# Kernel tuning notes

Hardware: AMD Instinct MI355X
Metric: run time of the kernel (lower is better)

## Reference

```python
import jax, jax.numpy as jnp
import numpy as np

VOCAB = 100000
EMBED = 128
B = 16384
W = 10  # context window size (indices fed as 'target' arg, per original naming)
K = 10  # number of negative samples


def setup_inputs() -> dict:
    key = jax.random.key(0)
    k1, k2, k3, k4 = jax.random.split(key, 4)
    initrange = 1.0 / EMBED
    # targetEmbedding: uniform(-1/D, 1/D); contextEmbedding: zeros (as in __init__).
    # Use small random values for contextEmbedding too so gradients/scores are non-trivial,
    # matching a mid-training state; math is identical.
    target_table = jax.random.uniform(k1, (VOCAB, EMBED), jnp.float32, -initrange, initrange)
    context_table = jax.random.uniform(k2, (VOCAB, EMBED), jnp.float32, -initrange, initrange)
    context = jax.random.randint(k3, (B,), 0, VOCAB)
    target = jax.random.randint(k4, (B, W), 0, VOCAB)
    negatives = jax.random.randint(jax.random.fold_in(key, 7), (B, K), 0, VOCAB)
    return {
        "target_table": target_table,
        "context_table": context_table,
        "context": context,
        "target": target,
        "negatives": negatives,
    }


def reference(target_table, context_table, context, target, negatives):
    # trg_embedding: gather window words then mean over window -> [B, D]
    trg = jnp.mean(target_table[target], axis=1)
    # center word embedding -> [B, D]
    ctx = context_table[context]
    # negatives embeddings -> [B, K, D]
    neg = context_table[negatives]

    pos_score = jnp.sum(trg * ctx, axis=1)                    # [B]
    pos_score = jnp.clip(pos_score, -10.0, 10.0)
    pos_loss = -jax.nn.log_sigmoid(pos_score)                 # [B]

    neg_score = jnp.einsum("bkd,bd->bk", neg, trg)           # [B, K]
    neg_score = jnp.clip(neg_score, -10.0, 10.0)
    neg_loss = -jnp.sum(jax.nn.log_sigmoid(-neg_score), axis=1)  # [B]

    return jnp.mean(pos_loss + neg_loss)
```

## Files before the change

### kernel.cpp

```cpp
#include <hip/hip_runtime.h>

#define VOCAB 100000
#define EMBED 128
#define BATCH 16384
#define WIN 10
#define NEG 10

__global__ __launch_bounds__(256) void cbow_loss_kernel(
    const float* __restrict__ target_table,
    const float* __restrict__ context_table,
    const int*   __restrict__ context,
    const int*   __restrict__ target,
    const int*   __restrict__ negatives,
    float*       __restrict__ out)
{
    const int tid    = threadIdx.x;
    const int lane16 = tid & 15;
    const int grp    = tid >> 4;
    const int b      = blockIdx.x * 16 + grp;

    const float4* tt4 = reinterpret_cast<const float4*>(target_table);
    const float4* ct4 = reinterpret_cast<const float4*>(context_table);
    const int lo = lane16 * 2;

    int tidx[WIN];
    #pragma unroll
    for (int w = 0; w < WIN; ++w) tidx[w] = target[b * WIN + w];
    const int cidx = context[b];
    int nidx[NEG];
    #pragma unroll
    for (int k = 0; k < NEG; ++k) nidx[k] = negatives[b * NEG + k];

    float4 t0 = make_float4(0.f, 0.f, 0.f, 0.f);
    float4 t1 = make_float4(0.f, 0.f, 0.f, 0.f);
    #pragma unroll
    for (int w = 0; w < WIN; ++w) {
        const float4* r = tt4 + (long long)tidx[w] * (EMBED / 4) + lo;
        const float4 a = r[0];
        const float4 c = r[1];
        t0.x += a.x; t0.y += a.y; t0.z += a.z; t0.w += a.w;
        t1.x += c.x; t1.y += c.y; t1.z += c.z; t1.w += c.w;
    }
    const float s = 1.0f / WIN;
    t0.x *= s; t0.y *= s; t0.z *= s; t0.w *= s;
    t1.x *= s; t1.y *= s; t1.z *= s; t1.w *= s;

    float sc[1 + NEG];
    {
        const float4* r = ct4 + (long long)cidx * (EMBED / 4) + lo;
        const float4 a = r[0];
        const float4 c = r[1];
        sc[0] = fmaf(t0.x, a.x, fmaf(t0.y, a.y, fmaf(t0.z, a.z, fmaf(t0.w, a.w,
                fmaf(t1.x, c.x, fmaf(t1.y, c.y, fmaf(t1.z, c.z, t1.w * c.w)))))));
    }
    #pragma unroll
    for (int k = 0; k < NEG; ++k) {
        const float4* r = ct4 + (long long)nidx[k] * (EMBED / 4) + lo;
        const float4 a = r[0];
        const float4 c = r[1];
        sc[1 + k] = fmaf(t0.x, a.x, fmaf(t0.y, a.y, fmaf(t0.z, a.z, fmaf(t0.w, a.w,
                    fmaf(t1.x, c.x, fmaf(t1.y, c.y, fmaf(t1.z, c.z, t1.w * c.w)))))));
    }

    #pragma unroll
    for (int off = 8; off >= 1; off >>= 1) {
        #pragma unroll
        for (int i = 0; i < 1 + NEG; ++i) sc[i] += __shfl_xor(sc[i], off, 16);
    }

    __shared__ float bsum;
    if (tid == 0) bsum = 0.f;
    __syncthreads();

    if (lane16 == 0) {
        float x = fminf(fmaxf(sc[0], -10.f), 10.f);
        float loss = log1pf(expf(-x));
        #pragma unroll
        for (int k = 0; k < NEG; ++k) {
            float y = fminf(fmaxf(sc[1 + k], -10.f), 10.f);
            loss += log1pf(expf(y));
        }
        atomicAdd(&bsum, loss);
    }
    __syncthreads();

    if (tid == 0) {
        atomicAdd(out, bsum * (1.0f / BATCH));
    }
}

extern "C" void kernel_launch(void* const* d_in, const int* in_sizes, int n_in,
                              void* d_out, int out_size, void* d_ws, size_t ws_size,
                              hipStream_t stream) {
    const float* target_table  = (const float*)d_in[0];
    const float* context_table = (const float*)d_in[1];
    const int*   context       = (const int*)d_in[2];
    const int*   target        = (const int*)d_in[3];
    const int*   negatives     = (const int*)d_in[4];
    float* out = (float*)d_out;

    hipMemsetAsync(out, 0, sizeof(float), stream);

    cbow_loss_kernel<<<BATCH / 16, 256, 0, stream>>>(
        target_table, context_table, context, target, negatives, out);
}
```

Before: 45.85 us.

## Use 32 lanes per row with one float4 each and shuffle-broadcast indices

Each batch row is now handled by 32 lanes, each loading one float4 per embedding row, instead of 16 lanes loading two float4s. The 21 indices per row are loaded cooperatively, one per lane, and broadcast with shuffles rather than every lane reading all of them. The grid doubles to 8 rows per block, and launch bounds now request a minimum occupancy. The intent is to raise memory-level parallelism and cut redundant index loads, at the cost of one extra shuffle-reduction step and twice as many per-block atomics.

```diff
diff --git a/kernel.cpp b/kernel.cpp
--- a/kernel.cpp
+++ b/kernel.cpp
@@ -6,7 +6,7 @@
 #define WIN 10
 #define NEG 10
 
-__global__ __launch_bounds__(256) void cbow_loss_kernel(
+__global__ __launch_bounds__(256, 4) void cbow_loss_kernel(
     const float* __restrict__ target_table,
     const float* __restrict__ context_table,
     const int*   __restrict__ context,
@@ -14,65 +14,57 @@
     const int*   __restrict__ negatives,
     float*       __restrict__ out)
 {
-    const int tid    = threadIdx.x;
-    const int lane16 = tid & 15;
-    const int grp    = tid >> 4;
-    const int b      = blockIdx.x * 16 + grp;
+    const int tid  = threadIdx.x;
+    const int lane = tid & 31;
+    const int grp  = tid >> 5;
+    const int b    = blockIdx.x * 8 + grp;
 
     const float4* tt4 = reinterpret_cast<const float4*>(target_table);
     const float4* ct4 = reinterpret_cast<const float4*>(context_table);
-    const int lo = lane16 * 2;
 
-    int tidx[WIN];
+    int myidx = 0;
+    if (lane < WIN)                 myidx = target[b * WIN + lane];
+    else if (lane == WIN)           myidx = context[b];
+    else if (lane < 2 * WIN + 1)    myidx = negatives[b * NEG + (lane - WIN - 1)];
+
+    int tidx[WIN], nidx[NEG];
     #pragma unroll
-    for (int w = 0; w < WIN; ++w) tidx[w] = target[b * WIN + w];
-    const int cidx = context[b];
-    int nidx[NEG];
+    for (int w = 0; w < WIN; ++w) tidx[w] = __shfl(myidx, w, 32);
+    const int cidx = __shfl(myidx, WIN, 32);
     #pragma unroll
-    for (int k = 0; k < NEG; ++k) nidx[k] = negatives[b * NEG + k];
+    for (int k = 0; k < NEG; ++k) nidx[k] = __shfl(myidx, WIN + 1 + k, 32);
 
-    float4 t0 = make_float4(0.f, 0.f, 0.f, 0.f);
-    float4 t1 = make_float4(0.f, 0.f, 0.f, 0.f);
+    float4 t = make_float4(0.f, 0.f, 0.f, 0.f);
     #pragma unroll
     for (int w = 0; w < WIN; ++w) {
-        const float4* r = tt4 + (long long)tidx[w] * (EMBED / 4) + lo;
-        const float4 a = r[0];
-        const float4 c = r[1];
-        t0.x += a.x; t0.y += a.y; t0.z += a.z; t0.w += a.w;
-        t1.x += c.x; t1.y += c.y; t1.z += c.z; t1.w += c.w;
+        const float4 v = tt4[(long long)tidx[w] * (EMBED / 4) + lane];
+        t.x += v.x; t.y += v.y; t.z += v.z; t.w += v.w;
     }
     const float s = 1.0f / WIN;
-    t0.x *= s; t0.y *= s; t0.z *= s; t0.w *= s;
-    t1.x *= s; t1.y *= s; t1.z *= s; t1.w *= s;
+    t.x *= s; t.y *= s; t.z *= s; t.w *= s;
 
     float sc[1 + NEG];
     {
-        const float4* r = ct4 + (long long)cidx * (EMBED / 4) + lo;
-        const float4 a = r[0];
-        const float4 c = r[1];
-        sc[0] = fmaf(t0.x, a.x, fmaf(t0.y, a.y, fmaf(t0.z, a.z, fmaf(t0.w, a.w,
-                fmaf(t1.x, c.x, fmaf(t1.y, c.y, fmaf(t1.z, c.z, t1.w * c.w)))))));
+        const float4 v = ct4[(long long)cidx * (EMBED / 4) + lane];
+        sc[0] = fmaf(t.x, v.x, fmaf(t.y, v.y, fmaf(t.z, v.z, t.w * v.w)));
     }
     #pragma unroll
     for (int k = 0; k < NEG; ++k) {
-        const float4* r = ct4 + (long long)nidx[k] * (EMBED / 4) + lo;
-        const float4 a = r[0];
-        const float4 c = r[1];
-        sc[1 + k] = fmaf(t0.x, a.x, fmaf(t0.y, a.y, fmaf(t0.z, a.z, fmaf(t0.w, a.w,
-                    fmaf(t1.x, c.x, fmaf(t1.y, c.y, fmaf(t1.z, c.z, t1.w * c.w)))))));
+        const float4 v = ct4[(long long)nidx[k] * (EMBED / 4) + lane];
+        sc[1 + k] = fmaf(t.x, v.x, fmaf(t.y, v.y, fmaf(t.z, v.z, t.w * v.w)));
     }
 
     #pragma unroll
-    for (int off = 8; off >= 1; off >>= 1) {
+    for (int off = 16; off >= 1; off >>= 1) {
         #pragma unroll
-        for (int i = 0; i < 1 + NEG; ++i) sc[i] += __shfl_xor(sc[i], off, 16);
+        for (int i = 0; i < 1 + NEG; ++i) sc[i] += __shfl_xor(sc[i], off, 32);
     }
 
     __shared__ float bsum;
     if (tid == 0) bsum = 0.f;
     __syncthreads();
 
-    if (lane16 == 0) {
+    if (lane == 0) {
         float x = fminf(fmaxf(sc[0], -10.f), 10.f);
         float loss = log1pf(expf(-x));
         #pragma unroll
@@ -101,6 +93,6 @@
 
     hipMemsetAsync(out, 0, sizeof(float), stream);
 
-    cbow_loss_kernel<<<BATCH / 16, 256, 0, stream>>>(
+    cbow_loss_kernel<<<BATCH / 8, 256, 0, stream>>>(
         target_table, context_table, context, target, negatives, out);
 }
```

Result: slower. 55.07 us (+20.1%).
